# Optimization experiments

Hardware: AMD Instinct MI355X
Metric: run time of the kernel (lower is better)

## Reference

```python
import jax, jax.numpy as jnp
import numpy as np

N_NODES = 50000
N_EDGES = 400000
N_GRAPHS = 512
IN_DIM = 768
HID = 64
BN_EPS = 1e-5


def setup_inputs() -> dict:
    key = jax.random.key(0)
    ks = jax.random.split(key, 12)
    x = jax.random.normal(ks[0], (N_NODES, IN_DIM), dtype=jnp.float32)
    edge_index = jax.random.randint(ks[1], (2, N_EDGES), 0, N_NODES, dtype=jnp.int64)
    batch = jnp.sort(jax.random.randint(ks[2], (N_NODES,), 0, N_GRAPHS, dtype=jnp.int64))

    def lin_init(k, fan_in, fan_out):
        kw, kb = jax.random.split(k)
        bound = 1.0 / np.sqrt(fan_in)
        W = jax.random.uniform(kw, (fan_in, fan_out), minval=-bound, maxval=bound, dtype=jnp.float32)
        b = jax.random.uniform(kb, (fan_out,), minval=-bound, maxval=bound, dtype=jnp.float32)
        return W, b

    w1a, b1a = lin_init(ks[3], IN_DIM, HID)
    w1b, b1b = lin_init(ks[4], HID, HID)
    w2a, b2a = lin_init(ks[5], HID, HID)
    w2b, b2b = lin_init(ks[6], HID, HID)
    wl, bl = lin_init(ks[7], 2 * HID, 2)

    ones = jnp.ones((HID,), jnp.float32)
    zeros = jnp.zeros((HID,), jnp.float32)
    return {
        "x": x, "edge_index": edge_index, "batch": batch,
        "w1a": w1a, "b1a": b1a, "g1": ones, "be1": zeros, "rm1": zeros, "rv1": ones,
        "w1b": w1b, "b1b": b1b,
        "w2a": w2a, "b2a": b2a, "g2": ones, "be2": zeros, "rm2": zeros, "rv2": ones,
        "w2b": w2b, "b2b": b2b,
        "wl": wl, "bl": bl,
    }


def _bn_eval(h, gamma, beta, rm, rv):
    # BatchNorm1d in eval mode: normalize with running stats
    return (h - rm) * (gamma * jax.lax.rsqrt(rv + BN_EPS)) + beta


def _gin_conv(x, src, dst, Wa, ba, gamma, beta, rm, rv, Wb, bb):
    # GINConv eps=0: h = MLP(x + sum_{j in N(i)} x_j); messages x[src] scatter-added to dst
    agg = jax.ops.segment_sum(x[src], dst, num_segments=N_NODES)
    h = x + agg
    h = jnp.dot(h, Wa) + ba
    h = jax.nn.relu(_bn_eval(h, gamma, beta, rm, rv))
    return jnp.dot(h, Wb) + bb


def reference(x, edge_index, batch,
              w1a, b1a, g1, be1, rm1, rv1, w1b, b1b,
              w2a, b2a, g2, be2, rm2, rv2, w2b, b2b,
              wl, bl):
    src, dst = edge_index[0], edge_index[1]
    # eval mode: dropout_edge and F.dropout are identity
    x1 = jax.nn.relu(_gin_conv(x, src, dst, w1a, b1a, g1, be1, rm1, rv1, w1b, b1b))
    x2 = jax.nn.relu(_gin_conv(x1, src, dst, w2a, b2a, g2, be2, rm2, rv2, w2b, b2b))
    x_jk = jnp.concatenate([x1, x2], axis=-1)  # [N, 2*HID]
    x_pool = jax.ops.segment_sum(x_jk, batch, num_segments=N_GRAPHS)  # [G, 2*HID]
    return jnp.dot(x_pool, wl) + bl  # [G, 2]
```

## Files before the change

### kernel.cpp

```cpp
#include <hip/hip_runtime.h>

constexpr int N_NODES  = 50000;
constexpr int N_EDGES  = 400000;
constexpr int N_GRAPHS = 512;
constexpr int IN_DIM   = 768;
constexpr int HID      = 64;
constexpr float BN_EPS = 1e-5f;
constexpr int CAP      = 64;

typedef __attribute__((ext_vector_type(8))) short bf16x8;
typedef __attribute__((ext_vector_type(4))) float f32x4;
typedef __attribute__((ext_vector_type(2))) float f32x2;

__device__ __forceinline__ unsigned int f2bf2(float lo, float hi) {
  unsigned int r;
  asm("v_cvt_pk_bf16_f32 %0, %1, %2" : "=v"(r) : "v"(lo), "v"(hi));
  return r;
}
__device__ __forceinline__ ushort f2bf1(float f) { return (ushort)f2bf2(f, f); }

__device__ __forceinline__ f32x2 unpk(unsigned int u) {
  f32x2 v;
  v.x = __uint_as_float(u << 16);
  v.y = __uint_as_float(u & 0xffff0000u);
  return v;
}

constexpr int WB_E = HID * HID;
constexpr int GB1  = (N_NODES + 127) / 128;
constexpr int BB   = (N_EDGES + 255) / 256;
constexpr int CVB  = (3 * WB_E) / 256;

__global__ __launch_bounds__(256) void gemm_build(
    const float* __restrict__ X, const float* __restrict__ w1a,
    ushort* __restrict__ P,
    const int* __restrict__ src, const int* __restrict__ dst,
    int* __restrict__ cnt, int* __restrict__ bucket,
    const float* __restrict__ w1b, const float* __restrict__ w2a,
    const float* __restrict__ w2b, const float* __restrict__ bl,
    ushort* __restrict__ WT1b, ushort* __restrict__ WT2a,
    ushort* __restrict__ WT2b, float* __restrict__ out) {
  const int tid = threadIdx.x;

  if (blockIdx.x >= GB1) {
    const int b = blockIdx.x - GB1;
    int e = b * 256 + tid;
    if (e < N_EDGES) {
      int s = src[e];
      int d = dst[e];
      int slot = atomicAdd(&cnt[d], 1);
      if (slot < CAP) bucket[d * CAP + slot] = s << 6;
    }
    if (b < CVB) {
      int j = b * 256 + tid;
      int w = j >> 12, r = j & (WB_E - 1);
      int c = r >> 6, k = r & 63;
      const float* W = (w == 0) ? w1b : (w == 1) ? w2a : w2b;
      ushort* D = (w == 0) ? WT1b : (w == 1) ? WT2a : WT2b;
      D[r] = f2bf1(W[k * HID + c]);
    } else if (b == CVB) {
      for (int o = tid; o < N_GRAPHS * 2; o += 256) out[o] = bl[o & 1];
    }
    return;
  }

  __shared__ ushort xs[2][128][64];
  __shared__ ushort ws[2][64][64];
  const int row0 = blockIdx.x * 128;
  const int wave = tid >> 6, lane = tid & 63, quad = lane >> 4, l16 = lane & 15;

  const int srow = tid >> 1;
  const int sk   = (tid & 1) * 32;
  int gr = row0 + srow;
  gr = gr < N_NODES ? gr : N_NODES - 1;
  const float* xrow = &X[(size_t)gr * IN_DIM + sk];
  const int wc  = tid & 63;
  const int wj0 = (tid >> 6) * 2;

  f32x4 acc[2][4] = {};

  float4 xv[8];
  float  wf[2][8];
#pragma unroll
  for (int i = 0; i < 8; i++) xv[i] = *(const float4*)&xrow[i * 4];
#pragma unroll
  for (int jj = 0; jj < 2; jj++)
#pragma unroll
    for (int i = 0; i < 8; i++)
      wf[jj][i] = w1a[((wj0 + jj) * 8 + i) * HID + wc];

  int t = 0;
  for (int kt = 0; kt < IN_DIM; kt += 64, t ^= 1) {
    unsigned int xw[16];
#pragma unroll
    for (int i = 0; i < 8; i++) {
      xw[i * 2 + 0] = f2bf2(xv[i].x, xv[i].y);
      xw[i * 2 + 1] = f2bf2(xv[i].z, xv[i].w);
    }
#pragma unroll
    for (int j = 0; j < 4; j++)
      *(uint4*)&xs[t][srow][(((sk >> 3) + j) ^ (srow & 7)) * 8] =
          *(const uint4*)&xw[j * 4];
#pragma unroll
    for (int jj = 0; jj < 2; jj++) {
      unsigned int pk[4];
#pragma unroll
      for (int q = 0; q < 4; q++) pk[q] = f2bf2(wf[jj][q * 2], wf[jj][q * 2 + 1]);
      *(uint4*)&ws[t][wc][((wj0 + jj) ^ (wc & 7)) * 8] = *(const uint4*)&pk[0];
    }

    if (kt + 64 < IN_DIM) {
#pragma unroll
      for (int i = 0; i < 8; i++) xv[i] = *(const float4*)&xrow[kt + 64 + i * 4];
#pragma unroll
      for (int jj = 0; jj < 2; jj++)
#pragma unroll
        for (int i = 0; i < 8; i++)
          wf[jj][i] = w1a[(kt + 64 + (wj0 + jj) * 8 + i) * HID + wc];
    }
    __syncthreads();

    const int ar0 = wave * 32 + l16;
    const int ar1 = ar0 + 16;
#pragma unroll
    for (int ks = 0; ks < 2; ks++) {
      bf16x8 a0 = *(const bf16x8*)&xs[t][ar0][((ks * 4 + quad) ^ (ar0 & 7)) * 8];
      bf16x8 a1 = *(const bf16x8*)&xs[t][ar1][((ks * 4 + quad) ^ (ar1 & 7)) * 8];
#pragma unroll
      for (int ct = 0; ct < 4; ct++) {
        const int br = ct * 16 + l16;
        bf16x8 b = *(const bf16x8*)&ws[t][br][((ks * 4 + quad) ^ (br & 7)) * 8];
        acc[0][ct] = __builtin_amdgcn_mfma_f32_16x16x32_bf16(a0, b, acc[0][ct], 0, 0, 0);
        acc[1][ct] = __builtin_amdgcn_mfma_f32_16x16x32_bf16(a1, b, acc[1][ct], 0, 0, 0);
      }
    }
  }

#pragma unroll
  for (int g2 = 0; g2 < 2; g2++)
#pragma unroll
    for (int ct = 0; ct < 4; ct++)
#pragma unroll
      for (int r = 0; r < 4; r++) {
        int row = row0 + wave * 32 + g2 * 16 + quad * 4 + r;
        if (row < N_NODES)
          P[(size_t)row * HID + ct * 16 + l16] = f2bf1(acc[g2][ct][r]);
      }
}

template <int CHAIN>
__global__ __launch_bounds__(256) void fused_mlp(
    const int* __restrict__ cnt, const int* __restrict__ bucket,
    const ushort* __restrict__ Pin,
    const float* __restrict__ bin, const float* __restrict__ g,
    const float* __restrict__ be, const float* __restrict__ rm,
    const float* __restrict__ rv,
    const ushort* __restrict__ WT1, const float* __restrict__ b1,
    const ushort* __restrict__ WT2, ushort* __restrict__ OUT2,
    const int* __restrict__ batch, const float* __restrict__ wlh,
    float* __restrict__ out) {
  __shared__ ushort xs[64][64];
  __shared__ ushort ws[64][64];
  __shared__ ushort ws2[CHAIN ? 64 : 1][64];
  __shared__ float sS[64], sT[64];
  __shared__ float gacc[64];
  __shared__ float wl_s[2 * HID];
  __shared__ int   sbatch[64];
  const int tid  = threadIdx.x;
  const int row0 = blockIdx.x * 64;
  const int srow = tid >> 2;
  const int sub  = tid & 3;
  const int qc0  = sub * 2;
  const int sub16 = sub * 16;

  int node = row0 + srow;
  node = node < N_NODES ? node : N_NODES - 1;
  const int c_raw = cnt[node];
  const int* bkt = &bucket[node * CAP];
  const int4 pre = *(const int4*)bkt;
  unsigned int sw[8];
  {
    const ushort* sp = &Pin[node * HID + sub16];
    *(uint4*)&sw[0] = *(const uint4*)&sp[0];
    *(uint4*)&sw[4] = *(const uint4*)&sp[8];
  }

  if (tid < 64) {
    int nb = row0 + tid;
    sbatch[tid] = batch[nb < N_NODES ? nb : N_NODES - 1];
    gacc[tid] = 0.0f;
    float s = g[tid] * rsqrtf(rv[tid] + BN_EPS);
    sS[tid] = s;
    sT[tid] = (bin[tid] - rm[tid]) * s + be[tid];
  }
  if (tid < 2 * HID) wl_s[tid] = wlh[tid];
  {
    uint4 w0 = *(const uint4*)&WT1[(size_t)srow * HID + qc0 * 8];
    uint4 w1 = *(const uint4*)&WT1[(size_t)srow * HID + qc0 * 8 + 8];
    *(uint4*)&ws[srow][((qc0 + 0) ^ (srow & 7)) * 8] = w0;
    *(uint4*)&ws[srow][((qc0 + 1) ^ (srow & 7)) * 8] = w1;
    if (CHAIN) {
      uint4 v0 = *(const uint4*)&WT2[(size_t)srow * HID + qc0 * 8];
      uint4 v1 = *(const uint4*)&WT2[(size_t)srow * HID + qc0 * 8 + 8];
      *(uint4*)&ws2[srow][((qc0 + 0) ^ (srow & 7)) * 8] = v0;
      *(uint4*)&ws2[srow][((qc0 + 1) ^ (srow & 7)) * 8] = v1;
    }
  }
  __syncthreads();

  const int g0 = sbatch[0], g1 = sbatch[63];
  const bool small = (g1 - g0) < 32;

  {
    f32x2 acc2[8];
#pragma unroll
    for (int j = 0; j < 8; j++) acc2[j] = unpk(sw[j]);

    int c = c_raw < CAP ? c_raw : CAP;
    int i = 0;
    if (c >= 4) {
      int4 s4 = pre;
      for (; i + 4 <= c; i += 4) {
        const int4 cur = s4;
        if (i + 8 <= c) s4 = *(const int4*)&bkt[i + 4];
        unsigned int w0[8], w1[8], w2[8], w3[8];
        const ushort* p0 = &Pin[cur.x + sub16];
        const ushort* p1 = &Pin[cur.y + sub16];
        const ushort* p2 = &Pin[cur.z + sub16];
        const ushort* p3 = &Pin[cur.w + sub16];
        *(uint4*)&w0[0] = *(const uint4*)&p0[0]; *(uint4*)&w0[4] = *(const uint4*)&p0[8];
        *(uint4*)&w1[0] = *(const uint4*)&p1[0]; *(uint4*)&w1[4] = *(const uint4*)&p1[8];
        *(uint4*)&w2[0] = *(const uint4*)&p2[0]; *(uint4*)&w2[4] = *(const uint4*)&p2[8];
        *(uint4*)&w3[0] = *(const uint4*)&p3[0]; *(uint4*)&w3[4] = *(const uint4*)&p3[8];
#pragma unroll
        for (int j = 0; j < 8; j++)
          acc2[j] += (unpk(w0[j]) + unpk(w1[j])) + (unpk(w2[j]) + unpk(w3[j]));
      }
    }
    for (; i < c; i++) {
      const ushort* p0 = &Pin[bkt[i] + sub16];
      unsigned int w0[8];
      *(uint4*)&w0[0] = *(const uint4*)&p0[0]; *(uint4*)&w0[4] = *(const uint4*)&p0[8];
#pragma unroll
      for (int j = 0; j < 8; j++) acc2[j] += unpk(w0[j]);
    }

    unsigned int hw[8];
#pragma unroll
    for (int j = 0; j < 8; j++) {
      const int col = sub16 + j * 2;
      float x0 = fmaxf(fmaf(acc2[j].x, sS[col],     sT[col]),     0.0f);
      float x1 = fmaxf(fmaf(acc2[j].y, sS[col + 1], sT[col + 1]), 0.0f);
      hw[j] = f2bf2(x0, x1);
    }
    *(uint4*)&xs[srow][((qc0 + 0) ^ (srow & 7)) * 8] = *(const uint4*)&hw[0];
    *(uint4*)&xs[srow][((qc0 + 1) ^ (srow & 7)) * 8] = *(const uint4*)&hw[4];
  }
  __syncthreads();

  const int wave = tid >> 6, lane = tid & 63, quad = lane >> 4, l16 = lane & 15;
  const int ar = wave * 16 + l16, axor = ar & 7;

  f32x4 acc1[4] = {};
#pragma unroll
  for (int ks = 0; ks < 2; ks++) {
    bf16x8 a = *(const bf16x8*)&xs[ar][((ks * 4 + quad) ^ axor) * 8];
#pragma unroll
    for (int ct = 0; ct < 4; ct++) {
      const int br = ct * 16 + l16;
      bf16x8 b = *(const bf16x8*)&ws[br][((ks * 4 + quad) ^ (br & 7)) * 8];
      acc1[ct] = __builtin_amdgcn_mfma_f32_16x16x32_bf16(a, b, acc1[ct], 0, 0, 0);
    }
  }

  if (CHAIN) __syncthreads();

  float v[4][4];
#pragma unroll
  for (int ct = 0; ct < 4; ct++) {
    const float bo = b1[ct * 16 + l16];
#pragma unroll
    for (int r = 0; r < 4; r++) v[ct][r] = fmaxf(acc1[ct][r] + bo, 0.0f);
  }

  {
    float p0[4] = {}, p1[4] = {};
#pragma unroll
    for (int ct = 0; ct < 4; ct++) {
      const int col = ct * 16 + l16;
      const float w0 = wl_s[col * 2 + 0], w1 = wl_s[col * 2 + 1];
#pragma unroll
      for (int r = 0; r < 4; r++) {
        p0[r] = fmaf(v[ct][r], w0, p0[r]);
        p1[r] = fmaf(v[ct][r], w1, p1[r]);
      }
    }
#pragma unroll
    for (int m = 1; m < 16; m <<= 1) {
#pragma unroll
      for (int r = 0; r < 4; r++) {
        p0[r] += __shfl_xor(p0[r], m);
        p1[r] += __shfl_xor(p1[r], m);
      }
    }
    if (l16 == 0) {
#pragma unroll
      for (int r = 0; r < 4; r++) {
        int lrow = wave * 16 + quad * 4 + r;
        if (row0 + lrow < N_NODES) {
          int gi = sbatch[lrow];
          if (small) {
            atomicAdd(&gacc[(gi - g0) * 2 + 0], p0[r]);
            atomicAdd(&gacc[(gi - g0) * 2 + 1], p1[r]);
          } else {
            atomicAdd(&out[gi * 2 + 0], p0[r]);
            atomicAdd(&out[gi * 2 + 1], p1[r]);
          }
        }
      }
    }
  }

  if (CHAIN) {
#pragma unroll
    for (int ct = 0; ct < 4; ct++) {
      const int col = ct * 16 + l16;
#pragma unroll
      for (int r = 0; r < 4; r++) {
        int lrow = wave * 16 + quad * 4 + r;
        xs[lrow][(((col >> 3) ^ (lrow & 7)) * 8) + (col & 7)] = f2bf1(v[ct][r]);
      }
    }
    __syncthreads();

    f32x4 accB[4] = {};
#pragma unroll
    for (int ks = 0; ks < 2; ks++) {
      bf16x8 a = *(const bf16x8*)&xs[ar][((ks * 4 + quad) ^ axor) * 8];
#pragma unroll
      for (int ct = 0; ct < 4; ct++) {
        const int br = ct * 16 + l16;
        bf16x8 b = *(const bf16x8*)&ws2[br][((ks * 4 + quad) ^ (br & 7)) * 8];
        accB[ct] = __builtin_amdgcn_mfma_f32_16x16x32_bf16(a, b, accB[ct], 0, 0, 0);
      }
    }
#pragma unroll
    for (int ct = 0; ct < 4; ct++) {
      const int col = ct * 16 + l16;
#pragma unroll
      for (int r = 0; r < 4; r++) {
        int grow = row0 + wave * 16 + quad * 4 + r;
        if (grow < N_NODES) OUT2[(size_t)grow * HID + col] = f2bf1(accB[ct][r]);
      }
    }
  }

  __syncthreads();
  if (small) {
    const int span2 = (g1 - g0 + 1) * 2;
    for (int z = tid; z < span2; z += 256) {
      float vv = gacc[z];
      if (vv != 0.0f) atomicAdd(&out[g0 * 2 + z], vv);
    }
  }
}

extern "C" void kernel_launch(void* const* d_in, const int* in_sizes, int n_in,
                              void* d_out, int out_size, void* d_ws, size_t ws_size,
                              hipStream_t stream) {
  const float* x   = (const float*)d_in[0];
  const int*   ei  = (const int*)d_in[1];
  const int*   bat = (const int*)d_in[2];
  const float* w1a = (const float*)d_in[3];
  const float* b1a = (const float*)d_in[4];
  const float* g1  = (const float*)d_in[5];
  const float* be1 = (const float*)d_in[6];
  const float* rm1 = (const float*)d_in[7];
  const float* rv1 = (const float*)d_in[8];
  const float* w1b = (const float*)d_in[9];
  const float* b1b = (const float*)d_in[10];
  const float* w2a = (const float*)d_in[11];
  const float* b2a = (const float*)d_in[12];
  const float* g2  = (const float*)d_in[13];
  const float* be2 = (const float*)d_in[14];
  const float* rm2 = (const float*)d_in[15];
  const float* rv2 = (const float*)d_in[16];
  const float* w2b = (const float*)d_in[17];
  const float* b2b = (const float*)d_in[18];
  const float* wl  = (const float*)d_in[19];
  const float* bl  = (const float*)d_in[20];
  float* out = (float*)d_out;

  const int* src = ei;
  const int* dst = ei + N_EDGES;

  const size_t FB = (size_t)N_NODES * HID;
  ushort* P1   = (ushort*)d_ws;
  ushort* P2   = P1 + FB;
  ushort* WT1b = P2 + FB;
  ushort* WT2a = WT1b + WB_E;
  ushort* WT2b = WT2a + WB_E;
  int* cnt     = (int*)(WT2b + WB_E);
  int* bucket  = cnt + N_NODES;

  const int GBF = (N_NODES + 63) / 64;

  hipMemsetAsync(cnt, 0, (size_t)N_NODES * sizeof(int), stream);
  gemm_build<<<GB1 + BB, 256, 0, stream>>>(x, w1a, P1, src, dst, cnt, bucket,
                                           w1b, w2a, w2b, bl,
                                           WT1b, WT2a, WT2b, out);
  fused_mlp<1><<<GBF, 256, 0, stream>>>(cnt, bucket, P1, b1a, g1, be1, rm1, rv1,
                                        WT1b, b1b, WT2a, P2, bat, wl, out);
  fused_mlp<0><<<GBF, 256, 0, stream>>>(cnt, bucket, P2, b2a, g2, be2, rm2, rv2,
                                        WT2b, b2b, nullptr, nullptr, bat,
                                        wl + 2 * HID, out);
}
```

Before: 307.7 us.

## Merge all phases into one cooperative persistent kernel with grid syncs

Replaces the memset plus three kernel launches with a single cooperative persistent kernel that runs init, GEMM/bucket build, and both MLP phases, separated by grid.sync, with blocks looping over tiles. The GEMM tile drops its double-buffered shared memory in favour of a single buffer with an extra barrier, which allows two blocks per CU. The aim is to remove launch gaps and tail effects between stages. In exchange the grid is capped by occupancy, per-tile setup is amortised but the loops add barriers, and a fallback multi-kernel path is kept in case the cooperative launch fails.

```diff
diff --git a/kernel.cpp b/kernel.cpp
--- a/kernel.cpp
+++ b/kernel.cpp
@@ -1,4 +1,7 @@
 #include <hip/hip_runtime.h>
+#include <hip/hip_cooperative_groups.h>
+
+namespace cg = cooperative_groups;
 
 constexpr int N_NODES  = 50000;
 constexpr int N_EDGES  = 400000;
@@ -29,44 +32,51 @@
 constexpr int WB_E = HID * HID;
 constexpr int GB1  = (N_NODES + 127) / 128;
 constexpr int BB   = (N_EDGES + 255) / 256;
-constexpr int CVB  = (3 * WB_E) / 256;
-
-__global__ __launch_bounds__(256) void gemm_build(
-    const float* __restrict__ X, const float* __restrict__ w1a,
-    ushort* __restrict__ P,
-    const int* __restrict__ src, const int* __restrict__ dst,
-    int* __restrict__ cnt, int* __restrict__ bucket,
-    const float* __restrict__ w1b, const float* __restrict__ w2a,
-    const float* __restrict__ w2b, const float* __restrict__ bl,
-    ushort* __restrict__ WT1b, ushort* __restrict__ WT2a,
-    ushort* __restrict__ WT2b, float* __restrict__ out) {
-  const int tid = threadIdx.x;
-
-  if (blockIdx.x >= GB1) {
-    const int b = blockIdx.x - GB1;
-    int e = b * 256 + tid;
-    if (e < N_EDGES) {
-      int s = src[e];
-      int d = dst[e];
-      int slot = atomicAdd(&cnt[d], 1);
-      if (slot < CAP) bucket[d * CAP + slot] = s << 6;
-    }
-    if (b < CVB) {
-      int j = b * 256 + tid;
-      int w = j >> 12, r = j & (WB_E - 1);
-      int c = r >> 6, k = r & 63;
-      const float* W = (w == 0) ? w1b : (w == 1) ? w2a : w2b;
-      ushort* D = (w == 0) ? WT1b : (w == 1) ? WT2a : WT2b;
-      D[r] = f2bf1(W[k * HID + c]);
-    } else if (b == CVB) {
-      for (int o = tid; o < N_GRAPHS * 2; o += 256) out[o] = bl[o & 1];
-    }
-    return;
-  }
-
-  __shared__ ushort xs[2][128][64];
-  __shared__ ushort ws[2][64][64];
-  const int row0 = blockIdx.x * 128;
+constexpr int GBF  = (N_NODES + 63) / 64;
+
+struct SMemG { ushort xs[128][64]; ushort ws[64][64]; };
+struct SMemM {
+  ushort xs[64][64];
+  ushort ws[64][64];
+  ushort ws2[64][64];
+  float sS[64], sT[64];
+  float gacc[64];
+  float wl_s[2 * HID];
+  int   sbatch[64];
+};
+union SMem { SMemG g; SMemM m; };
+
+struct Params {
+  const float* x;
+  const int*   src;
+  const int*   dst;
+  const int*   bat;
+  const float *w1a, *w1b, *w2a, *w2b;
+  const float *b1a, *g1, *be1, *rm1, *rv1, *b1b;
+  const float *b2a, *g2, *be2, *rm2, *rv2, *b2b;
+  const float *wl, *bl;
+  ushort *P1, *P2, *WT1b, *WT2a, *WT2b;
+  int    *cnt, *bucket;
+  float  *out;
+};
+
+__device__ __forceinline__ void init_work(const Params& p, int gthr, int nthr) {
+  for (int i = gthr; i < N_NODES; i += nthr) p.cnt[i] = 0;
+  for (int j = gthr; j < 3 * WB_E; j += nthr) {
+    int w = j >> 12, r = j & (WB_E - 1);
+    int c = r >> 6, k = r & 63;
+    const float* W = (w == 0) ? p.w1b : (w == 1) ? p.w2a : p.w2b;
+    ushort* D = (w == 0) ? p.WT1b : (w == 1) ? p.WT2a : p.WT2b;
+    D[r] = f2bf1(W[k * HID + c]);
+  }
+  for (int o = gthr; o < N_GRAPHS * 2; o += nthr) p.out[o] = p.bl[o & 1];
+}
+
+__device__ __forceinline__ void gemm_tile(SMemG& sm, int tile,
+                                          const float* __restrict__ X,
+                                          const float* __restrict__ w1a,
+                                          ushort* __restrict__ P, int tid) {
+  const int row0 = tile * 128;
   const int wave = tid >> 6, lane = tid & 63, quad = lane >> 4, l16 = lane & 15;
 
   const int srow = tid >> 1;
@@ -78,7 +88,6 @@
   const int wj0 = (tid >> 6) * 2;
 
   f32x4 acc[2][4] = {};
-
   float4 xv[8];
   float  wf[2][8];
 #pragma unroll
@@ -89,8 +98,7 @@
     for (int i = 0; i < 8; i++)
       wf[jj][i] = w1a[((wj0 + jj) * 8 + i) * HID + wc];
 
-  int t = 0;
-  for (int kt = 0; kt < IN_DIM; kt += 64, t ^= 1) {
+  for (int kt = 0; kt < IN_DIM; kt += 64) {
     unsigned int xw[16];
 #pragma unroll
     for (int i = 0; i < 8; i++) {
@@ -99,14 +107,14 @@
     }
 #pragma unroll
     for (int j = 0; j < 4; j++)
-      *(uint4*)&xs[t][srow][(((sk >> 3) + j) ^ (srow & 7)) * 8] =
+      *(uint4*)&sm.xs[srow][(((sk >> 3) + j) ^ (srow & 7)) * 8] =
           *(const uint4*)&xw[j * 4];
 #pragma unroll
     for (int jj = 0; jj < 2; jj++) {
       unsigned int pk[4];
 #pragma unroll
       for (int q = 0; q < 4; q++) pk[q] = f2bf2(wf[jj][q * 2], wf[jj][q * 2 + 1]);
-      *(uint4*)&ws[t][wc][((wj0 + jj) ^ (wc & 7)) * 8] = *(const uint4*)&pk[0];
+      *(uint4*)&sm.ws[wc][((wj0 + jj) ^ (wc & 7)) * 8] = *(const uint4*)&pk[0];
     }
 
     if (kt + 64 < IN_DIM) {
@@ -124,16 +132,17 @@
     const int ar1 = ar0 + 16;
 #pragma unroll
     for (int ks = 0; ks < 2; ks++) {
-      bf16x8 a0 = *(const bf16x8*)&xs[t][ar0][((ks * 4 + quad) ^ (ar0 & 7)) * 8];
-      bf16x8 a1 = *(const bf16x8*)&xs[t][ar1][((ks * 4 + quad) ^ (ar1 & 7)) * 8];
+      bf16x8 a0 = *(const bf16x8*)&sm.xs[ar0][((ks * 4 + quad) ^ (ar0 & 7)) * 8];
+      bf16x8 a1 = *(const bf16x8*)&sm.xs[ar1][((ks * 4 + quad) ^ (ar1 & 7)) * 8];
 #pragma unroll
       for (int ct = 0; ct < 4; ct++) {
         const int br = ct * 16 + l16;
-        bf16x8 b = *(const bf16x8*)&ws[t][br][((ks * 4 + quad) ^ (br & 7)) * 8];
+        bf16x8 b = *(const bf16x8*)&sm.ws[br][((ks * 4 + quad) ^ (br & 7)) * 8];
         acc[0][ct] = __builtin_amdgcn_mfma_f32_16x16x32_bf16(a0, b, acc[0][ct], 0, 0, 0);
         acc[1][ct] = __builtin_amdgcn_mfma_f32_16x16x32_bf16(a1, b, acc[1][ct], 0, 0, 0);
       }
     }
+    __syncthreads();
   }
 
 #pragma unroll
@@ -148,270 +157,339 @@
       }
 }
 
+__device__ __forceinline__ void build_chunk(int b, const Params& p, int tid) {
+  int e = b * 256 + tid;
+  if (e < N_EDGES) {
+    int s = p.src[e];
+    int d = p.dst[e];
+    int slot = atomicAdd(&p.cnt[d], 1);
+    if (slot < CAP) p.bucket[d * CAP + slot] = s << 6;
+  }
+}
+
 template <int CHAIN>
-__global__ __launch_bounds__(256) void fused_mlp(
-    const int* __restrict__ cnt, const int* __restrict__ bucket,
+__device__ __forceinline__ void mlp_phase(
+    SMemM& sm, const int* __restrict__ cnt, const int* __restrict__ bucket,
     const ushort* __restrict__ Pin,
-    const float* __restrict__ bin, const float* __restrict__ g,
+    const float* __restrict__ bin, const float* __restrict__ gam,
     const float* __restrict__ be, const float* __restrict__ rm,
     const float* __restrict__ rv,
     const ushort* __restrict__ WT1, const float* __restrict__ b1,
     const ushort* __restrict__ WT2, ushort* __restrict__ OUT2,
     const int* __restrict__ batch, const float* __restrict__ wlh,
-    float* __restrict__ out) {
-  __shared__ ushort xs[64][64];
-  __shared__ ushort ws[64][64];
-  __shared__ ushort ws2[CHAIN ? 64 : 1][64];
-  __shared__ float sS[64], sT[64];
-  __shared__ float gacc[64];
-  __shared__ float wl_s[2 * HID];
-  __shared__ int   sbatch[64];
-  const int tid  = threadIdx.x;
-  const int row0 = blockIdx.x * 64;
-  const int srow = tid >> 2;
-  const int sub  = tid & 3;
-  const int qc0  = sub * 2;
+    float* __restrict__ out, int tid, int bid, int stride) {
+  const int srow  = tid >> 2;
+  const int sub   = tid & 3;
+  const int qc0   = sub * 2;
   const int sub16 = sub * 16;
 
-  int node = row0 + srow;
-  node = node < N_NODES ? node : N_NODES - 1;
-  const int c_raw = cnt[node];
-  const int* bkt = &bucket[node * CAP];
-  const int4 pre = *(const int4*)bkt;
-  unsigned int sw[8];
-  {
-    const ushort* sp = &Pin[node * HID + sub16];
-    *(uint4*)&sw[0] = *(const uint4*)&sp[0];
-    *(uint4*)&sw[4] = *(const uint4*)&sp[8];
-  }
-
   if (tid < 64) {
-    int nb = row0 + tid;
-    sbatch[tid] = batch[nb < N_NODES ? nb : N_NODES - 1];
-    gacc[tid] = 0.0f;
-    float s = g[tid] * rsqrtf(rv[tid] + BN_EPS);
-    sS[tid] = s;
-    sT[tid] = (bin[tid] - rm[tid]) * s + be[tid];
-  }
-  if (tid < 2 * HID) wl_s[tid] = wlh[tid];
+    float s = gam[tid] * rsqrtf(rv[tid] + BN_EPS);
+    sm.sS[tid] = s;
+    sm.sT[tid] = (bin[tid] - rm[tid]) * s + be[tid];
+  }
+  if (tid < 2 * HID) sm.wl_s[tid] = wlh[tid];
   {
     uint4 w0 = *(const uint4*)&WT1[(size_t)srow * HID + qc0 * 8];
     uint4 w1 = *(const uint4*)&WT1[(size_t)srow * HID + qc0 * 8 + 8];
-    *(uint4*)&ws[srow][((qc0 + 0) ^ (srow & 7)) * 8] = w0;
-    *(uint4*)&ws[srow][((qc0 + 1) ^ (srow & 7)) * 8] = w1;
+    *(uint4*)&sm.ws[srow][((qc0 + 0) ^ (srow & 7)) * 8] = w0;
+    *(uint4*)&sm.ws[srow][((qc0 + 1) ^ (srow & 7)) * 8] = w1;
     if (CHAIN) {
       uint4 v0 = *(const uint4*)&WT2[(size_t)srow * HID + qc0 * 8];
       uint4 v1 = *(const uint4*)&WT2[(size_t)srow * HID + qc0 * 8 + 8];
-      *(uint4*)&ws2[srow][((qc0 + 0) ^ (srow & 7)) * 8] = v0;
-      *(uint4*)&ws2[srow][((qc0 + 1) ^ (srow & 7)) * 8] = v1;
-    }
-  }
-  __syncthreads();
-
-  const int g0 = sbatch[0], g1 = sbatch[63];
-  const bool small = (g1 - g0) < 32;
-
-  {
-    f32x2 acc2[8];
-#pragma unroll
-    for (int j = 0; j < 8; j++) acc2[j] = unpk(sw[j]);
-
-    int c = c_raw < CAP ? c_raw : CAP;
-    int i = 0;
-    if (c >= 4) {
-      int4 s4 = pre;
-      for (; i + 4 <= c; i += 4) {
-        const int4 cur = s4;
-        if (i + 8 <= c) s4 = *(const int4*)&bkt[i + 4];
-        unsigned int w0[8], w1[8], w2[8], w3[8];
-        const ushort* p0 = &Pin[cur.x + sub16];
-        const ushort* p1 = &Pin[cur.y + sub16];
-        const ushort* p2 = &Pin[cur.z + sub16];
-        const ushort* p3 = &Pin[cur.w + sub16];
-        *(uint4*)&w0[0] = *(const uint4*)&p0[0]; *(uint4*)&w0[4] = *(const uint4*)&p0[8];
-        *(uint4*)&w1[0] = *(const uint4*)&p1[0]; *(uint4*)&w1[4] = *(const uint4*)&p1[8];
-        *(uint4*)&w2[0] = *(const uint4*)&p2[0]; *(uint4*)&w2[4] = *(const uint4*)&p2[8];
-        *(uint4*)&w3[0] = *(const uint4*)&p3[0]; *(uint4*)&w3[4] = *(const uint4*)&p3[8];
-#pragma unroll
-        for (int j = 0; j < 8; j++)
-          acc2[j] += (unpk(w0[j]) + unpk(w1[j])) + (unpk(w2[j]) + unpk(w3[j]));
-      }
-    }
-    for (; i < c; i++) {
-      const ushort* p0 = &Pin[bkt[i] + sub16];
-      unsigned int w0[8];
-      *(uint4*)&w0[0] = *(const uint4*)&p0[0]; *(uint4*)&w0[4] = *(const uint4*)&p0[8];
-#pragma unroll
-      for (int j = 0; j < 8; j++) acc2[j] += unpk(w0[j]);
-    }
-
-    unsigned int hw[8];
-#pragma unroll
-    for (int j = 0; j < 8; j++) {
-      const int col = sub16 + j * 2;
-      float x0 = fmaxf(fmaf(acc2[j].x, sS[col],     sT[col]),     0.0f);
-      float x1 = fmaxf(fmaf(acc2[j].y, sS[col + 1], sT[col + 1]), 0.0f);
-      hw[j] = f2bf2(x0, x1);
-    }
-    *(uint4*)&xs[srow][((qc0 + 0) ^ (srow & 7)) * 8] = *(const uint4*)&hw[0];
-    *(uint4*)&xs[srow][((qc0 + 1) ^ (srow & 7)) * 8] = *(const uint4*)&hw[4];
+      *(uint4*)&sm.ws2[srow][((qc0 + 0) ^ (srow & 7)) * 8] = v0;
+      *(uint4*)&sm.ws2[srow][((qc0 + 1) ^ (srow & 7)) * 8] = v1;
+    }
   }
   __syncthreads();
 
   const int wave = tid >> 6, lane = tid & 63, quad = lane >> 4, l16 = lane & 15;
   const int ar = wave * 16 + l16, axor = ar & 7;
 
-  f32x4 acc1[4] = {};
-#pragma unroll
-  for (int ks = 0; ks < 2; ks++) {
-    bf16x8 a = *(const bf16x8*)&xs[ar][((ks * 4 + quad) ^ axor) * 8];
-#pragma unroll
-    for (int ct = 0; ct < 4; ct++) {
-      const int br = ct * 16 + l16;
-      bf16x8 b = *(const bf16x8*)&ws[br][((ks * 4 + quad) ^ (br & 7)) * 8];
-      acc1[ct] = __builtin_amdgcn_mfma_f32_16x16x32_bf16(a, b, acc1[ct], 0, 0, 0);
-    }
-  }
-
-  if (CHAIN) __syncthreads();
-
-  float v[4][4];
-#pragma unroll
-  for (int ct = 0; ct < 4; ct++) {
-    const float bo = b1[ct * 16 + l16];
-#pragma unroll
-    for (int r = 0; r < 4; r++) v[ct][r] = fmaxf(acc1[ct][r] + bo, 0.0f);
-  }
-
-  {
-    float p0[4] = {}, p1[4] = {};
-#pragma unroll
-    for (int ct = 0; ct < 4; ct++) {
-      const int col = ct * 16 + l16;
-      const float w0 = wl_s[col * 2 + 0], w1 = wl_s[col * 2 + 1];
-#pragma unroll
-      for (int r = 0; r < 4; r++) {
-        p0[r] = fmaf(v[ct][r], w0, p0[r]);
-        p1[r] = fmaf(v[ct][r], w1, p1[r]);
-      }
-    }
-#pragma unroll
-    for (int m = 1; m < 16; m <<= 1) {
-#pragma unroll
-      for (int r = 0; r < 4; r++) {
-        p0[r] += __shfl_xor(p0[r], m);
-        p1[r] += __shfl_xor(p1[r], m);
-      }
-    }
-    if (l16 == 0) {
-#pragma unroll
-      for (int r = 0; r < 4; r++) {
-        int lrow = wave * 16 + quad * 4 + r;
-        if (row0 + lrow < N_NODES) {
-          int gi = sbatch[lrow];
-          if (small) {
-            atomicAdd(&gacc[(gi - g0) * 2 + 0], p0[r]);
-            atomicAdd(&gacc[(gi - g0) * 2 + 1], p1[r]);
-          } else {
-            atomicAdd(&out[gi * 2 + 0], p0[r]);
-            atomicAdd(&out[gi * 2 + 1], p1[r]);
-          }
-        }
-      }
-    }
-  }
-
-  if (CHAIN) {
-#pragma unroll
-    for (int ct = 0; ct < 4; ct++) {
-      const int col = ct * 16 + l16;
-#pragma unroll
-      for (int r = 0; r < 4; r++) {
-        int lrow = wave * 16 + quad * 4 + r;
-        xs[lrow][(((col >> 3) ^ (lrow & 7)) * 8) + (col & 7)] = f2bf1(v[ct][r]);
-      }
+  for (int t = bid; t < GBF; t += stride) {
+    const int row0 = t * 64;
+
+    int node = row0 + srow;
+    node = node < N_NODES ? node : N_NODES - 1;
+    const int c_raw = cnt[node];
+    const int* bkt = &bucket[node * CAP];
+    const int4 pre = *(const int4*)bkt;
+    unsigned int sw[8];
+    {
+      const ushort* sp = &Pin[node * HID + sub16];
+      *(uint4*)&sw[0] = *(const uint4*)&sp[0];
+      *(uint4*)&sw[4] = *(const uint4*)&sp[8];
+    }
+    if (tid < 64) {
+      int nb = row0 + tid;
+      sm.sbatch[tid] = batch[nb < N_NODES ? nb : N_NODES - 1];
+      sm.gacc[tid] = 0.0f;
+    }
+
+    {
+      f32x2 acc2[8];
+#pragma unroll
+      for (int j = 0; j < 8; j++) acc2[j] = unpk(sw[j]);
+
+      int c = c_raw < CAP ? c_raw : CAP;
+      int i = 0;
+      if (c >= 4) {
+        int4 s4 = pre;
+        for (; i + 4 <= c; i += 4) {
+          const int4 cur = s4;
+          if (i + 8 <= c) s4 = *(const int4*)&bkt[i + 4];
+          unsigned int w0[8], w1[8], w2[8], w3[8];
+          const ushort* p0 = &Pin[cur.x + sub16];
+          const ushort* p1 = &Pin[cur.y + sub16];
+          const ushort* p2 = &Pin[cur.z + sub16];
+          const ushort* p3 = &Pin[cur.w + sub16];
+          *(uint4*)&w0[0] = *(const uint4*)&p0[0]; *(uint4*)&w0[4] = *(const uint4*)&p0[8];
+          *(uint4*)&w1[0] = *(const uint4*)&p1[0]; *(uint4*)&w1[4] = *(const uint4*)&p1[8];
+          *(uint4*)&w2[0] = *(const uint4*)&p2[0]; *(uint4*)&w2[4] = *(const uint4*)&p2[8];
+          *(uint4*)&w3[0] = *(const uint4*)&p3[0]; *(uint4*)&w3[4] = *(const uint4*)&p3[8];
+#pragma unroll
+          for (int j = 0; j < 8; j++)
+            acc2[j] += (unpk(w0[j]) + unpk(w1[j])) + (unpk(w2[j]) + unpk(w3[j]));
+        }
+      }
+      for (; i < c; i++) {
+        const ushort* p0 = &Pin[bkt[i] + sub16];
+        unsigned int w0[8];
+        *(uint4*)&w0[0] = *(const uint4*)&p0[0]; *(uint4*)&w0[4] = *(const uint4*)&p0[8];
+#pragma unroll
+        for (int j = 0; j < 8; j++) acc2[j] += unpk(w0[j]);
+      }
+
+      unsigned int hw[8];
+#pragma unroll
+      for (int j = 0; j < 8; j++) {
+        const int col = sub16 + j * 2;
+        float x0 = fmaxf(fmaf(acc2[j].x, sm.sS[col],     sm.sT[col]),     0.0f);
+        float x1 = fmaxf(fmaf(acc2[j].y, sm.sS[col + 1], sm.sT[col + 1]), 0.0f);
+        hw[j] = f2bf2(x0, x1);
+      }
+      *(uint4*)&sm.xs[srow][((qc0 + 0) ^ (srow & 7)) * 8] = *(const uint4*)&hw[0];
+      *(uint4*)&sm.xs[srow][((qc0 + 1) ^ (srow & 7)) * 8] = *(const uint4*)&hw[4];
     }
     __syncthreads();
 
-    f32x4 accB[4] = {};
+    const int g0 = sm.sbatch[0], g1v = sm.sbatch[63];
+    const bool small = (g1v - g0) < 32;
+
+    f32x4 acc1[4] = {};
 #pragma unroll
     for (int ks = 0; ks < 2; ks++) {
-      bf16x8 a = *(const bf16x8*)&xs[ar][((ks * 4 + quad) ^ axor) * 8];
+      bf16x8 a = *(const bf16x8*)&sm.xs[ar][((ks * 4 + quad) ^ axor) * 8];
 #pragma unroll
       for (int ct = 0; ct < 4; ct++) {
         const int br = ct * 16 + l16;
-        bf16x8 b = *(const bf16x8*)&ws2[br][((ks * 4 + quad) ^ (br & 7)) * 8];
-        accB[ct] = __builtin_amdgcn_mfma_f32_16x16x32_bf16(a, b, accB[ct], 0, 0, 0);
-      }
-    }
+        bf16x8 b = *(const bf16x8*)&sm.ws[br][((ks * 4 + quad) ^ (br & 7)) * 8];
+        acc1[ct] = __builtin_amdgcn_mfma_f32_16x16x32_bf16(a, b, acc1[ct], 0, 0, 0);
+      }
+    }
+
+    if (CHAIN) __syncthreads();
+
+    float v[4][4];
 #pragma unroll
     for (int ct = 0; ct < 4; ct++) {
-      const int col = ct * 16 + l16;
-#pragma unroll
-      for (int r = 0; r < 4; r++) {
-        int grow = row0 + wave * 16 + quad * 4 + r;
-        if (grow < N_NODES) OUT2[(size_t)grow * HID + col] = f2bf1(accB[ct][r]);
-      }
-    }
-  }
-
-  __syncthreads();
-  if (small) {
-    const int span2 = (g1 - g0 + 1) * 2;
-    for (int z = tid; z < span2; z += 256) {
-      float vv = gacc[z];
-      if (vv != 0.0f) atomicAdd(&out[g0 * 2 + z], vv);
-    }
-  }
+      const float bo = b1[ct * 16 + l16];
+#pragma unroll
+      for (int r = 0; r < 4; r++) v[ct][r] = fmaxf(acc1[ct][r] + bo, 0.0f);
+    }
+
+    {
+      float p0[4] = {}, p1[4] = {};
+#pragma unroll
+      for (int ct = 0; ct < 4; ct++) {
+        const int col = ct * 16 + l16;
+        const float w0 = sm.wl_s[col * 2 + 0], w1 = sm.wl_s[col * 2 + 1];
+#pragma unroll
+        for (int r = 0; r < 4; r++) {
+          p0[r] = fmaf(v[ct][r], w0, p0[r]);
+          p1[r] = fmaf(v[ct][r], w1, p1[r]);
+        }
+      }
+#pragma unroll
+      for (int m = 1; m < 16; m <<= 1) {
+#pragma unroll
+        for (int r = 0; r < 4; r++) {
+          p0[r] += __shfl_xor(p0[r], m);
+          p1[r] += __shfl_xor(p1[r], m);
+        }
+      }
+      if (l16 == 0) {
+#pragma unroll
+        for (int r = 0; r < 4; r++) {
+          int lrow = wave * 16 + quad * 4 + r;
+          if (row0 + lrow < N_NODES) {
+            int gi = sm.sbatch[lrow];
+            if (small) {
+              atomicAdd(&sm.gacc[(gi - g0) * 2 + 0], p0[r]);
+              atomicAdd(&sm.gacc[(gi - g0) * 2 + 1], p1[r]);
+            } else {
+              atomicAdd(&out[gi * 2 + 0], p0[r]);
+              atomicAdd(&out[gi * 2 + 1], p1[r]);
+            }
+          }
+        }
+      }
+    }
+
+    if (CHAIN) {
+#pragma unroll
+      for (int ct = 0; ct < 4; ct++) {
+        const int col = ct * 16 + l16;
+#pragma unroll
+        for (int r = 0; r < 4; r++) {
+          int lrow = wave * 16 + quad * 4 + r;
+          sm.xs[lrow][(((col >> 3) ^ (lrow & 7)) * 8) + (col & 7)] = f2bf1(v[ct][r]);
+        }
+      }
+      __syncthreads();
+
+      f32x4 accB[4] = {};
+#pragma unroll
+      for (int ks = 0; ks < 2; ks++) {
+        bf16x8 a = *(const bf16x8*)&sm.xs[ar][((ks * 4 + quad) ^ axor) * 8];
+#pragma unroll
+        for (int ct = 0; ct < 4; ct++) {
+          const int br = ct * 16 + l16;
+          bf16x8 b = *(const bf16x8*)&sm.ws2[br][((ks * 4 + quad) ^ (br & 7)) * 8];
+          accB[ct] = __builtin_amdgcn_mfma_f32_16x16x32_bf16(a, b, accB[ct], 0, 0, 0);
+        }
+      }
+#pragma unroll
+      for (int ct = 0; ct < 4; ct++) {
+        const int col = ct * 16 + l16;
+#pragma unroll
+        for (int r = 0; r < 4; r++) {
+          int grow = row0 + wave * 16 + quad * 4 + r;
+          if (grow < N_NODES) OUT2[(size_t)grow * HID + col] = f2bf1(accB[ct][r]);
+        }
+      }
+    }
+
+    __syncthreads();
+    if (small) {
+      const int span2 = (g1v - g0 + 1) * 2;
+      for (int z = tid; z < span2; z += 256) {
+        float vv = sm.gacc[z];
+        if (vv != 0.0f) atomicAdd(&out[g0 * 2 + z], vv);
+      }
+    }
+    __syncthreads();
+  }
+}
+
+__global__ __launch_bounds__(256, 2) void mega(Params p) {
+  __shared__ SMem sm;
+  cg::grid_group grid = cg::this_grid();
+  const int tid  = threadIdx.x;
+  const int bid  = blockIdx.x;
+  const int nb   = gridDim.x;
+  const int nthr = nb * 256;
+
+  init_work(p, bid * 256 + tid, nthr);
+  grid.sync();
+
+  for (int item = bid; item < GB1 + BB; item += nb) {
+    if (item < GB1) gemm_tile(sm.g, item, p.x, p.w1a, p.P1, tid);
+    else            build_chunk(item - GB1, p, tid);
+  }
+  grid.sync();
+
+  mlp_phase<1>(sm.m, p.cnt, p.bucket, p.P1, p.b1a, p.g1, p.be1, p.rm1, p.rv1,
+               p.WT1b, p.b1b, p.WT2a, p.P2, p.bat, p.wl, p.out, tid, bid, nb);
+  grid.sync();
+
+  mlp_phase<0>(sm.m, p.cnt, p.bucket, p.P2, p.b2a, p.g2, p.be2, p.rm2, p.rv2,
+               p.WT2b, p.b2b, nullptr, nullptr, p.bat, p.wl + 2 * HID, p.out,
+               tid, bid, nb);
+}
+
+__global__ __launch_bounds__(256) void init_k(Params p) {
+  init_work(p, blockIdx.x * 256 + threadIdx.x, gridDim.x * 256);
+}
+__global__ __launch_bounds__(256) void gb_k(Params p) {
+  __shared__ SMemG smg;
+  if (blockIdx.x < GB1) gemm_tile(smg, blockIdx.x, p.x, p.w1a, p.P1, threadIdx.x);
+  else                  build_chunk(blockIdx.x - GB1, p, threadIdx.x);
+}
+template <int CHAIN>
+__global__ __launch_bounds__(256) void mlp_k(Params p) {
+  __shared__ SMemM smm;
+  if (CHAIN)
+    mlp_phase<1>(smm, p.cnt, p.bucket, p.P1, p.b1a, p.g1, p.be1, p.rm1, p.rv1,
+                 p.WT1b, p.b1b, p.WT2a, p.P2, p.bat, p.wl, p.out,
+                 threadIdx.x, blockIdx.x, gridDim.x);
+  else
+    mlp_phase<0>(smm, p.cnt, p.bucket, p.P2, p.b2a, p.g2, p.be2, p.rm2, p.rv2,
+                 p.WT2b, p.b2b, nullptr, nullptr, p.bat, p.wl + 2 * HID, p.out,
+                 threadIdx.x, blockIdx.x, gridDim.x);
 }
 
 extern "C" void kernel_launch(void* const* d_in, const int* in_sizes, int n_in,
                               void* d_out, int out_size, void* d_ws, size_t ws_size,
                               hipStream_t stream) {
-  const float* x   = (const float*)d_in[0];
-  const int*   ei  = (const int*)d_in[1];
-  const int*   bat = (const int*)d_in[2];
-  const float* w1a = (const float*)d_in[3];
-  const float* b1a = (const float*)d_in[4];
-  const float* g1  = (const float*)d_in[5];
-  const float* be1 = (const float*)d_in[6];
-  const float* rm1 = (const float*)d_in[7];
-  const float* rv1 = (const float*)d_in[8];
-  const float* w1b = (const float*)d_in[9];
-  const float* b1b = (const float*)d_in[10];
-  const float* w2a = (const float*)d_in[11];
-  const float* b2a = (const float*)d_in[12];
-  const float* g2  = (const float*)d_in[13];
-  const float* be2 = (const float*)d_in[14];
-  const float* rm2 = (const float*)d_in[15];
-  const float* rv2 = (const float*)d_in[16];
-  const float* w2b = (const float*)d_in[17];
-  const float* b2b = (const float*)d_in[18];
-  const float* wl  = (const float*)d_in[19];
-  const float* bl  = (const float*)d_in[20];
-  float* out = (float*)d_out;
-
-  const int* src = ei;
-  const int* dst = ei + N_EDGES;
+  Params p;
+  p.x   = (const float*)d_in[0];
+  const int* ei = (const int*)d_in[1];
+  p.src = ei;
+  p.dst = ei + N_EDGES;
+  p.bat = (const int*)d_in[2];
+  p.w1a = (const float*)d_in[3];
+  p.b1a = (const float*)d_in[4];
+  p.g1  = (const float*)d_in[5];
+  p.be1 = (const float*)d_in[6];
+  p.rm1 = (const float*)d_in[7];
+  p.rv1 = (const float*)d_in[8];
+  p.w1b = (const float*)d_in[9];
+  p.b1b = (const float*)d_in[10];
+  p.w2a = (const float*)d_in[11];
+  p.b2a = (const float*)d_in[12];
+  p.g2  = (const float*)d_in[13];
+  p.be2 = (const float*)d_in[14];
+  p.rm2 = (const float*)d_in[15];
+  p.rv2 = (const float*)d_in[16];
+  p.w2b = (const float*)d_in[17];
+  p.b2b = (const float*)d_in[18];
+  p.wl  = (const float*)d_in[19];
+  p.bl  = (const float*)d_in[20];
+  p.out = (float*)d_out;
 
   const size_t FB = (size_t)N_NODES * HID;
-  ushort* P1   = (ushort*)d_ws;
-  ushort* P2   = P1 + FB;
-  ushort* WT1b = P2 + FB;
-  ushort* WT2a = WT1b + WB_E;
-  ushort* WT2b = WT2a + WB_E;
-  int* cnt     = (int*)(WT2b + WB_E);
-  int* bucket  = cnt + N_NODES;
-
-  const int GBF = (N_NODES + 63) / 64;
-
-  hipMemsetAsync(cnt, 0, (size_t)N_NODES * sizeof(int), stream);
-  gemm_build<<<GB1 + BB, 256, 0, stream>>>(x, w1a, P1, src, dst, cnt, bucket,
-                                           w1b, w2a, w2b, bl,
-                                           WT1b, WT2a, WT2b, out);
-  fused_mlp<1><<<GBF, 256, 0, stream>>>(cnt, bucket, P1, b1a, g1, be1, rm1, rv1,
-                                        WT1b, b1b, WT2a, P2, bat, wl, out);
-  fused_mlp<0><<<GBF, 256, 0, stream>>>(cnt, bucket, P2, b2a, g2, be2, rm2, rv2,
-                                        WT2b, b2b, nullptr, nullptr, bat,
-                                        wl + 2 * HID, out);
-}
+  p.P1     = (ushort*)d_ws;
+  p.P2     = p.P1 + FB;
+  p.WT1b   = p.P2 + FB;
+  p.WT2a   = p.WT1b + WB_E;
+  p.WT2b   = p.WT2a + WB_E;
+  p.cnt    = (int*)(p.WT2b + WB_E);
+  p.bucket = p.cnt + N_NODES;
+
+  static int coop_grid = -1;
+  if (coop_grid < 0) {
+    int maxb = 0;
+    hipDeviceProp_t prop{};
+    if (hipOccupancyMaxActiveBlocksPerMultiprocessor(
+            &maxb, (const void*)mega, 256, 0) == hipSuccess &&
+        hipGetDeviceProperties(&prop, 0) == hipSuccess && maxb > 0)
+      coop_grid = maxb * prop.multiProcessorCount;
+    else
+      coop_grid = 0;
+  }
+
+  if (coop_grid > 0) {
+    int nblk = coop_grid < 2048 ? coop_grid : 2048;
+    void* kargs[] = { (void*)&p };
+    if (hipLaunchCooperativeKernel((const void*)mega, dim3(nblk), dim3(256),
+                                   kargs, 0, stream) == hipSuccess)
+      return;
+    coop_grid = 0;
+  }
+
+  init_k<<<(N_NODES + 255) / 256, 256, 0, stream>>>(p);
+  gb_k<<<GB1 + BB, 256, 0, stream>>>(p);
+  mlp_k<1><<<GBF, 256, 0, stream>>>(p);
+  mlp_k<0><<<GBF, 256, 0, stream>>>(p);
+}
```

New measurement: 464.7 us. 1.51x slower.
